# Kernel optimization log

Measured on AMD Instinct MI355X. Metric: run time of the kernel, lower is better.

## Reference

```python
import jax, jax.numpy as jnp
import numpy as np
from jax import lax

HIDDEN_DIM = 32
MLP_INNER = 8
VOCAB_SIZE = 64
INFERENCE_LR = 0.01
THRESHOLD = 4.0
B, L = 256, 4096
LN_EPS = 1e-5


def setup_inputs() -> dict:
    key = jax.random.key(0)
    ks = jax.random.split(key, 14)
    s = 0.1
    f32 = jnp.float32
    return {
        "seq": jax.random.randint(ks[0], (B, L), 0, VOCAB_SIZE),
        "embed": (jax.random.normal(ks[1], (VOCAB_SIZE, HIDDEN_DIM)) * s).astype(f32),
        "ff1_w": (jax.random.normal(ks[2], (2 * HIDDEN_DIM, HIDDEN_DIM)) * s).astype(f32),
        "ff1_b": jnp.zeros((2 * HIDDEN_DIM,), f32),
        "ff2_w": (jax.random.normal(ks[3], (HIDDEN_DIM, 2 * HIDDEN_DIM)) * s).astype(f32),
        "ff2_b": jnp.zeros((HIDDEN_DIM,), f32),
        "ln_g": jnp.ones((HIDDEN_DIM,), f32),
        "ln_b": jnp.zeros((HIDDEN_DIM,), f32),
        "fc1_w": (jax.random.normal(ks[4], (MLP_INNER, HIDDEN_DIM)) * s).astype(f32),
        "fc1_b": jnp.zeros((MLP_INNER,), f32),
        "fc2_w": (jax.random.normal(ks[5], (HIDDEN_DIM, MLP_INNER)) * s).astype(f32),
        "fc2_b": jnp.zeros((HIDDEN_DIM,), f32),
        "out_w": (jax.random.normal(ks[6], (VOCAB_SIZE, HIDDEN_DIM)) * s).astype(f32),
        "out_b": jnp.zeros((VOCAB_SIZE,), f32),
    }


def _encoder(seq, embed, ff1_w, ff1_b, ff2_w, ff2_b, ln_g, ln_b):
    h = embed[seq]  # [B, L, H]
    z = jax.nn.relu(jnp.einsum('blh,kh->blk', h, ff1_w) + ff1_b)
    f = jnp.einsum('blk,hk->blh', z, ff2_w) + ff2_b
    x = h + f
    mu = x.mean(-1, keepdims=True)
    var = ((x - mu) ** 2).mean(-1, keepdims=True)
    return ln_g * (x - mu) * lax.rsqrt(var + LN_EPS) + ln_b


def _fast_weight_scan(keys, vals, query, fc1_w, fc1_b, fc2_w, fc2_b):
    # keys, vals: [n_steps, H] for one sample; query: [H]
    H = keys.shape[-1]

    def step(carry, kv):
        W1, b1, W2, b2, ssum, cnt = carry
        k, v = kv
        mean_h = ssum / jnp.maximum(cnt, 1.0)
        dist = jnp.sqrt(jnp.sum((k - mean_h) ** 2))
        write = jnp.logical_or(cnt == 0.0, dist > THRESHOLD)
        # forward of tiny MLP on key
        z1 = W1 @ k + b1
        a = jax.nn.relu(z1)
        pred = W2 @ a + b2
        # MSE (mean over H) gradient, manual SGD step
        dpred = (2.0 / H) * (pred - v)
        dW2 = jnp.outer(dpred, a)
        db2 = dpred
        dz1 = (W2.T @ dpred) * (z1 > 0)
        dW1 = jnp.outer(dz1, k)
        db1 = dz1
        lr = INFERENCE_LR
        W1n = jnp.where(write, W1 - lr * dW1, W1)
        b1n = jnp.where(write, b1 - lr * db1, b1)
        W2n = jnp.where(write, W2 - lr * dW2, W2)
        b2n = jnp.where(write, b2 - lr * db2, b2)
        return (W1n, b1n, W2n, b2n, ssum + k, cnt + 1.0), write

    carry0 = (fc1_w, fc1_b, fc2_w, fc2_b, jnp.zeros_like(query), jnp.asarray(0.0, query.dtype))
    (W1, b1, W2, b2, _, _), writes = lax.scan(step, carry0, (keys, vals))
    context = W2 @ jax.nn.relu(W1 @ query + b1) + b2
    return context, writes.sum()


def reference(seq, embed, ff1_w, ff1_b, ff2_w, ff2_b, ln_g, ln_b,
              fc1_w, fc1_b, fc2_w, fc2_b, out_w, out_b):
    hidden = _encoder(seq, embed, ff1_w, ff1_b, ff2_w, ff2_b, ln_g, ln_b)
    hidden = lax.stop_gradient(hidden)  # inner loop uses detached hiddens
    Lseq = hidden.shape[1]
    n = (Lseq - 3 + 1) // 2  # len(range(0, L-3, 2))
    keys = hidden[:, 0:2 * n:2, :]   # [B, n, H]
    vals = hidden[:, 1:2 * n:2, :]   # [B, n, H]
    query = hidden[:, -1, :]          # [B, H]
    ctx, n_writes = jax.vmap(_fast_weight_scan, in_axes=(0, 0, 0, None, None, None, None))(
        keys, vals, query, fc1_w, fc1_b, fc2_w, fc2_b)
    ctx = lax.stop_gradient(ctx)  # torch computes context under no_grad
    logits = ctx @ out_w.T + out_b  # [B, VOCAB]
    write_rate = n_writes.sum().astype(jnp.float32) / (hidden.shape[0] * n)
    return logits, write_rate
```

## Files before the change

kernel.cpp:

```cpp
#include <hip/hip_runtime.h>

#define L_SEQ 4096
#define NSTEP 2047
#define ST_W  (-0.000625f)


__device__ __forceinline__ void redi4(float& a, float& b, float& c, float& d) {
    asm volatile(
        "s_nop 1\n\t"
        "v_add_f32_dpp %0, %0, %0 quad_perm:[1,0,3,2] row_mask:0xf bank_mask:0xf bound_ctrl:0\n\t"
        "v_add_f32_dpp %1, %1, %1 quad_perm:[1,0,3,2] row_mask:0xf bank_mask:0xf bound_ctrl:0\n\t"
        "v_add_f32_dpp %2, %2, %2 quad_perm:[1,0,3,2] row_mask:0xf bank_mask:0xf bound_ctrl:0\n\t"
        "v_add_f32_dpp %3, %3, %3 quad_perm:[1,0,3,2] row_mask:0xf bank_mask:0xf bound_ctrl:0\n\t"
        "v_add_f32_dpp %0, %0, %0 quad_perm:[2,3,0,1] row_mask:0xf bank_mask:0xf bound_ctrl:0\n\t"
        "v_add_f32_dpp %1, %1, %1 quad_perm:[2,3,0,1] row_mask:0xf bank_mask:0xf bound_ctrl:0\n\t"
        "v_add_f32_dpp %2, %2, %2 quad_perm:[2,3,0,1] row_mask:0xf bank_mask:0xf bound_ctrl:0\n\t"
        "v_add_f32_dpp %3, %3, %3 quad_perm:[2,3,0,1] row_mask:0xf bank_mask:0xf bound_ctrl:0\n\t"
        "v_add_f32_dpp %0, %0, %0 row_half_mirror row_mask:0xf bank_mask:0xf bound_ctrl:0\n\t"
        "v_add_f32_dpp %1, %1, %1 row_half_mirror row_mask:0xf bank_mask:0xf bound_ctrl:0\n\t"
        "v_add_f32_dpp %2, %2, %2 row_half_mirror row_mask:0xf bank_mask:0xf bound_ctrl:0\n\t"
        "v_add_f32_dpp %3, %3, %3 row_half_mirror row_mask:0xf bank_mask:0xf bound_ctrl:0"
        : "+v"(a), "+v"(b), "+v"(c), "+v"(d));
}

__device__ __forceinline__ float redg1(float x) {
    float t;
    asm volatile(
        "s_nop 1\n\t"
        "v_add_f32_dpp %0, %0, %0 row_ror:8 row_mask:0xf bank_mask:0xf bound_ctrl:0\n\t"
        "s_nop 1\n\t"
        "v_mov_b32 %1, %0\n\t"
        "s_nop 1\n\t"
        "v_permlane16_swap_b32 %1, %0\n\t"
        "s_nop 0\n\t"
        "v_add_f32 %0, %0, %1\n\t"
        "s_nop 1\n\t"
        "v_mov_b32 %1, %0\n\t"
        "s_nop 1\n\t"
        "v_permlane32_swap_b32 %1, %0\n\t"
        "s_nop 0\n\t"
        "v_add_f32 %0, %0, %1"
        : "+v"(x), "=&v"(t));
    return x;
}

__device__ __forceinline__ float sel8u(const float* Z, int r) {
    unsigned long long m0 = (r & 1) ? ~0ull : 0ull;
    unsigned long long m1 = (r & 2) ? ~0ull : 0ull;
    unsigned long long m2 = (r & 4) ? ~0ull : 0ull;
    float a0, a1, a2, a3, b0, b1v, res;
    asm("v_cndmask_b32 %0, %1, %2, %3" : "=v"(a0) : "v"(Z[0]), "v"(Z[1]), "s"(m0));
    asm("v_cndmask_b32 %0, %1, %2, %3" : "=v"(a1) : "v"(Z[2]), "v"(Z[3]), "s"(m0));
    asm("v_cndmask_b32 %0, %1, %2, %3" : "=v"(a2) : "v"(Z[4]), "v"(Z[5]), "s"(m0));
    asm("v_cndmask_b32 %0, %1, %2, %3" : "=v"(a3) : "v"(Z[6]), "v"(Z[7]), "s"(m0));
    asm("v_cndmask_b32 %0, %1, %2, %3" : "=v"(b0)  : "v"(a0), "v"(a1), "s"(m1));
    asm("v_cndmask_b32 %0, %1, %2, %3" : "=v"(b1v) : "v"(a2), "v"(a3), "s"(m1));
    asm("v_cndmask_b32 %0, %1, %2, %3" : "=v"(res) : "v"(b0), "v"(b1v), "s"(m2));
    return res;
}

__device__ __forceinline__ float bperm_row(int tok, int i4, float v) {
    int addr = ((tok & 56) << 2) | i4;
    return __int_as_float(__builtin_amdgcn_ds_bpermute(addr, __float_as_int(v)));
}

__device__ __forceinline__ int rli(int x, int l) {
    return __builtin_amdgcn_readlane(x, l);
}

__global__ __launch_bounds__(64) void build_kernel(
    const float* __restrict__ embed, const float* __restrict__ ff1_w,
    const float* __restrict__ ff1_b, const float* __restrict__ ff2_w,
    const float* __restrict__ ff2_b, const float* __restrict__ ln_g,
    const float* __restrict__ ln_b, const float* __restrict__ fc1_w,
    float* __restrict__ table, float* __restrict__ G, float* __restrict__ Z0)
{
    __shared__ float tl[64][32];
    const int v = threadIdx.x;
    float h[32], f[32];
#pragma unroll
    for (int j = 0; j < 32; ++j) { h[j] = embed[v * 32 + j]; f[j] = 0.f; }
    for (int k = 0; k < 64; ++k) {
        float z = ff1_b[k];
#pragma unroll
        for (int j = 0; j < 32; ++j) z += h[j] * ff1_w[k * 32 + j];
        z = fmaxf(z, 0.f);
#pragma unroll
        for (int j = 0; j < 32; ++j) f[j] += z * ff2_w[j * 64 + k];
    }
    float x[32], mu = 0.f;
#pragma unroll
    for (int j = 0; j < 32; ++j) { x[j] = h[j] + f[j] + ff2_b[j]; mu += x[j]; }
    mu *= (1.f / 32.f);
    float var = 0.f;
#pragma unroll
    for (int j = 0; j < 32; ++j) { float d = x[j] - mu; var += d * d; }
    var *= (1.f / 32.f);
    const float inv = rsqrtf(var + 1e-5f);
    float tv[32];
#pragma unroll
    for (int j = 0; j < 32; ++j) {
        tv[j] = ln_g[j] * (x[j] - mu) * inv + ln_b[j];
        tl[v][j] = tv[j];
        table[v * 32 + j] = tv[j];
    }
    __syncthreads();
    for (int u = 0; u < 64; ++u) {
        float acc = 0.f;
#pragma unroll
        for (int j = 0; j < 32; ++j) acc += tv[j] * tl[u][j];
        G[v * 64 + u] = acc;
    }
    for (int i = 0; i < 8; ++i) {
        float acc = 0.f;
#pragma unroll
        for (int j = 0; j < 32; ++j) acc += fc1_w[i * 32 + j] * tv[j];
        Z0[v * 8 + i] = acc;
    }
}

__global__ __launch_bounds__(256) void flags_kernel(
    const int* __restrict__ seq, const float* __restrict__ Gg,
    unsigned int* __restrict__ flags, float* __restrict__ wacc)
{
    __shared__ float Gs[4096];
    __shared__ float P[64][64];
    __shared__ int   kt[2048];
    __shared__ float Aa[2048];
    __shared__ float Ws[2048];
    __shared__ float red[256];
    const int tid = threadIdx.x, b = blockIdx.x;
    for (int idx = tid; idx < 4096; idx += 256) Gs[idx] = Gg[idx];
    const int2* sp2 = reinterpret_cast<const int2*>(seq + b * L_SEQ);
    for (int j = tid; j < 2048; j += 256) kt[j] = sp2[j].x;
    __syncthreads();

    for (int idx = tid; idx < 4096; idx += 256) {
        const int c = idx >> 6, u = idx & 63;
        const int base = c * 32;
        float s = 0.f;
#pragma unroll 4
        for (int j = 0; j < 32; ++j) s += Gs[kt[base + j] * 64 + u];
        P[c][u] = s;
    }
    __syncthreads();
    if (tid < 64) {
        float acc = 0.f;
        for (int c = 0; c < 64; ++c) { float p = P[c][tid]; P[c][tid] = acc; acc += p; }
    }
    __syncthreads();
    for (int t = tid; t < NSTEP; t += 256) {
        const int c = t >> 5, base = c << 5;
        const int ktt = kt[t];
        float a = P[c][ktt];
        for (int s = base; s < t; ++s) a += Gs[kt[s] * 64 + ktt];
        Aa[t] = a;
        Ws[t] = 2.f * a + Gs[ktt * 65];
    }
    __syncthreads();
    float loc[8], tot = 0.f;
    const int base8 = tid * 8;
#pragma unroll
    for (int j = 0; j < 8; ++j) {
        float v = (base8 + j < NSTEP) ? Ws[base8 + j] : 0.f;
        loc[j] = tot; tot += v;
    }
    red[tid] = tot;
    __syncthreads();
    float run = tot;
    for (int off = 1; off < 256; off <<= 1) {
        float add = (tid >= off) ? red[tid - off] : 0.f;
        __syncthreads();
        run += add; red[tid] = run;
        __syncthreads();
    }
    const float excl = run - tot;
    __syncthreads();
#pragma unroll
    for (int j = 0; j < 8; ++j) {
        const int t = base8 + j;
        if (t < NSTEP) {
            const float u_t = excl + loc[j];
            const float tf = (float)t;
            const int ktt = kt[t];
            const float r = fmaf(tf * tf, Gs[ktt * 65] - 16.f, u_t)
                            - 2.f * tf * Aa[t];
            Ws[t] = (t == 0 || r > 0.f) ? 1.f : 0.f;
        }
    }
    __syncthreads();
    int cnt = 0;
    if (tid < 64) {
        unsigned int w = 0;
        for (int j = 0; j < 32; ++j) {
            const int t = tid * 32 + j;
            if (t < NSTEP && Ws[t] != 0.f) w |= 1u << j;
        }
        flags[b * 64 + tid] = w;
        cnt = __popc(w);
    }
    red[tid] = (float)cnt;
    __syncthreads();
    if (tid == 0) {
        float s = 0.f;
        for (int j = 0; j < 64; ++j) s += red[j];
        atomicAdd(wacc, s);
    }
}

__global__ __launch_bounds__(64) void scan_kernel(
    const int* __restrict__ seq, const float* __restrict__ tableg,
    const float* __restrict__ Gg, const float* __restrict__ Z0g,
    const float* __restrict__ fc1_b, const float* __restrict__ fc2_w,
    const float* __restrict__ fc2_b, const float* __restrict__ out_w,
    const float* __restrict__ out_b, const unsigned int* __restrict__ flags,
    const float* __restrict__ wacc, float* __restrict__ out)
{
    __shared__ float Gs[4096];
    __shared__ float tabs[2048];
    __shared__ float ctx_s[32];
    const int b = blockIdx.x, tid = threadIdx.x;
    const int i = tid & 7, g = tid >> 3;
    const int l31 = tid & 31;
    const int i4 = i << 2;

    if (b == 0 && tid == 0) out[16384] = wacc[0] * (1.0f / 524032.0f);

    for (int idx = tid; idx < 4096; idx += 64) Gs[idx] = Gg[idx];
    for (int idx = tid; idx < 2048; idx += 64) tabs[idx] = tableg[idx];
    __syncthreads();
    const float4* tab4 = reinterpret_cast<const float4*>(tabs);

    float Zr[8];
#pragma unroll
    for (int r = 0; r < 8; ++r) Zr[r] = Z0g[(8 * g + r) * 8 + i];
    float b1 = fc1_b[i];
    float W2r0 = fc2_w[(4 * g + 0) * 8 + i];
    float W2r1 = fc2_w[(4 * g + 1) * 8 + i];
    float W2r2 = fc2_w[(4 * g + 2) * 8 + i];
    float W2r3 = fc2_w[(4 * g + 3) * 8 + i];
    float4 b2r = reinterpret_cast<const float4*>(fc2_b)[g];

    const int2* sp2 = reinterpret_cast<const int2*>(seq + b * L_SEQ);
    const unsigned int fwv = flags[b * 64 + tid];

    int2 cbA = sp2[l31];
    int2 cbB = sp2[32 + l31];
    int2 cbC = sp2[64 + l31];

    int k0t = rli(cbA.x, 0);
    int v0t = rli(cbA.y, 0);
    int kn1 = rli(cbA.x, 1);
    int vn1 = rli(cbA.y, 1);

    const float4* gp0 = reinterpret_cast<const float4*>(Gs + k0t * 64 + 8 * g);
    float4 GaC = gp0[0], GbC = gp0[1];
    float4 vc0 = tab4[v0t * 8 + g];
    float gbIn = Gs[k0t * 64 + kn1];
    float yb = bperm_row(k0t, i4, sel8u(Zr, k0t & 7)) + b1;
    float es0 = b2r.x - vc0.x, es1 = b2r.y - vc0.y;
    float es2 = b2r.z - vc0.z, es3 = b2r.w - vc0.w;
    float c_prev = 0.f, gB1c = 0.f;

    for (int c = 0; c < 64; ++c) {
        const unsigned int fw = (unsigned int)rli((int)fwv, c);
        {
            int c2 = c + 2; if (c2 > 63) c2 = 63;
            int2 t2 = sp2[c2 * 32 + l31];
            cbC = t2;
        }
#pragma unroll
        for (int j = 0; j < 32; ++j) {
            int kn2, vn2;
            if (j < 30) { kn2 = rli(cbA.x, j + 2); vn2 = rli(cbA.y, j + 2); }
            else        { kn2 = rli(cbB.x, j - 30); vn2 = rli(cbB.y, j - 30); }
            const float st = ((fw >> j) & 1u) ? ST_W : 0.f;

            float ynv = bperm_row(kn1, i4, sel8u(Zr, kn1 & 7));

            const float4* gpn =
                reinterpret_cast<const float4*>(Gs + kn1 * 64 + 8 * g);
            float4 GaN = gpn[0], GbN = gpn[1];
            float4 vcN = tab4[vn1 * 8 + g];
            float gbNew = Gs[kn1 * 64 + kn2];

            const float z1 = fmaf(c_prev, gB1c, yb);
            const float a  = fmaxf(z1, 0.f);
            float p0 = W2r0 * a, p1 = W2r1 * a, p2 = W2r2 * a, p3 = W2r3 * a;
            redi4(p0, p1, p2, p3);
            const float dp0 = p0 + es0, dp1 = p1 + es1;
            const float dp2 = p2 + es2, dp3 = p3 + es3;
            float q = redg1(fmaf(W2r0, dp0, W2r1 * dp1) +
                            fmaf(W2r2, dp2, W2r3 * dp3));
            const float cc = (z1 > 0.f) ? st * q : 0.f;

            const float u0 = st * dp0, u1 = st * dp1;
            const float u2 = st * dp2, u3 = st * dp3;
            W2r0 = fmaf(u0, a, W2r0); W2r1 = fmaf(u1, a, W2r1);
            W2r2 = fmaf(u2, a, W2r2); W2r3 = fmaf(u3, a, W2r3);
            b2r.x += u0; b2r.y += u1; b2r.z += u2; b2r.w += u3;
            Zr[0] = fmaf(cc, GaC.x, Zr[0]); Zr[1] = fmaf(cc, GaC.y, Zr[1]);
            Zr[2] = fmaf(cc, GaC.z, Zr[2]); Zr[3] = fmaf(cc, GaC.w, Zr[3]);
            Zr[4] = fmaf(cc, GbC.x, Zr[4]); Zr[5] = fmaf(cc, GbC.y, Zr[5]);
            Zr[6] = fmaf(cc, GbC.z, Zr[6]); Zr[7] = fmaf(cc, GbC.w, Zr[7]);
            const float ybN = ynv + b1;
            b1 += cc;
            es0 = b2r.x - vcN.x; es1 = b2r.y - vcN.y;
            es2 = b2r.z - vcN.z; es3 = b2r.w - vcN.w;

            yb = ybN; c_prev = cc; gB1c = gbIn + 1.f; gbIn = gbNew;
            GaC = GaN; GbC = GbN;
            kn1 = kn2; vn1 = vn2;
        }
        cbA = cbB; cbB = cbC;
    }

    const int tq = seq[b * L_SEQ + (L_SEQ - 1)];
    float yq = bperm_row(tq, i4, sel8u(Zr, tq & 7));
    const float zq = yq + b1;
    const float aq = fmaxf(zq, 0.f);
    float c0 = W2r0 * aq, c1 = W2r1 * aq, c2 = W2r2 * aq, c3 = W2r3 * aq;
    redi4(c0, c1, c2, c3);
    if (i == 0) {
        ctx_s[4 * g + 0] = c0 + b2r.x;
        ctx_s[4 * g + 1] = c1 + b2r.y;
        ctx_s[4 * g + 2] = c2 + b2r.z;
        ctx_s[4 * g + 3] = c3 + b2r.w;
    }
    __syncthreads();

    float acc = out_b[tid];
#pragma unroll
    for (int j = 0; j < 32; ++j) acc += ctx_s[j] * out_w[tid * 32 + j];
    out[b * 64 + tid] = acc;
}

extern "C" void kernel_launch(void* const* d_in, const int* in_sizes, int n_in,
                              void* d_out, int out_size, void* d_ws, size_t ws_size,
                              hipStream_t stream)
{
    const int*   seq   = (const int*)  d_in[0];
    const float* embed = (const float*)d_in[1];
    const float* ff1_w = (const float*)d_in[2];
    const float* ff1_b = (const float*)d_in[3];
    const float* ff2_w = (const float*)d_in[4];
    const float* ff2_b = (const float*)d_in[5];
    const float* ln_g  = (const float*)d_in[6];
    const float* ln_b  = (const float*)d_in[7];
    const float* fc1_w = (const float*)d_in[8];
    const float* fc1_b = (const float*)d_in[9];
    const float* fc2_w = (const float*)d_in[10];
    const float* fc2_b = (const float*)d_in[11];
    const float* out_w = (const float*)d_in[12];
    const float* out_b = (const float*)d_in[13];

    float* out = (float*)d_out;
    char* ws = (char*)d_ws;
    float*        table = (float*)(ws + 0);
    float*        G     = (float*)(ws + 8192);
    float*        Z0    = (float*)(ws + 24576);
    float*        wacc  = (float*)(ws + 26624);
    unsigned int* flags = (unsigned int*)(ws + 28672);

    hipMemsetAsync(wacc, 0, sizeof(float), stream);
    hipLaunchKernelGGL(build_kernel, dim3(1), dim3(64), 0, stream,
                       embed, ff1_w, ff1_b, ff2_w, ff2_b, ln_g, ln_b, fc1_w,
                       table, G, Z0);
    hipLaunchKernelGGL(flags_kernel, dim3(256), dim3(256), 0, stream,
                       seq, G, flags, wacc);
    hipLaunchKernelGGL(scan_kernel, dim3(256), dim3(64), 0, stream,
                       seq, table, G, Z0, fc1_b, fc2_w, fc2_b,
                       out_w, out_b, flags, wacc, out);
}
```

Before: 472.3 us.

## Fuse table/Gram build into flags kernel and shorten scan prefetch distance

Removes the single-block build kernel and has every flags_kernel block recompute the 64-entry LayerNorm table and the Gram matrix in shared memory, with block 0 writing table, G and Z0 to global memory for the scan kernel. This drops one serial launch that ran on a single wave and the global reload of G. The scan loop's lookahead on next token ids is cut from two steps to one, which removes a carried register pair but exposes the LDS loads for the next step with less lead time. Each flags block now repeats the small encoder MLP work, adding redundant compute per block.

```diff
diff --git a/kernel.cpp b/kernel.cpp
--- a/kernel.cpp
+++ b/kernel.cpp
@@ -68,71 +68,74 @@
     return __builtin_amdgcn_readlane(x, l);
 }
 
-__global__ __launch_bounds__(64) void build_kernel(
-    const float* __restrict__ embed, const float* __restrict__ ff1_w,
-    const float* __restrict__ ff1_b, const float* __restrict__ ff2_w,
-    const float* __restrict__ ff2_b, const float* __restrict__ ln_g,
-    const float* __restrict__ ln_b, const float* __restrict__ fc1_w,
-    float* __restrict__ table, float* __restrict__ G, float* __restrict__ Z0)
-{
-    __shared__ float tl[64][32];
-    const int v = threadIdx.x;
-    float h[32], f[32];
-#pragma unroll
-    for (int j = 0; j < 32; ++j) { h[j] = embed[v * 32 + j]; f[j] = 0.f; }
-    for (int k = 0; k < 64; ++k) {
-        float z = ff1_b[k];
-#pragma unroll
-        for (int j = 0; j < 32; ++j) z += h[j] * ff1_w[k * 32 + j];
-        z = fmaxf(z, 0.f);
-#pragma unroll
-        for (int j = 0; j < 32; ++j) f[j] += z * ff2_w[j * 64 + k];
-    }
-    float x[32], mu = 0.f;
-#pragma unroll
-    for (int j = 0; j < 32; ++j) { x[j] = h[j] + f[j] + ff2_b[j]; mu += x[j]; }
-    mu *= (1.f / 32.f);
-    float var = 0.f;
-#pragma unroll
-    for (int j = 0; j < 32; ++j) { float d = x[j] - mu; var += d * d; }
-    var *= (1.f / 32.f);
-    const float inv = rsqrtf(var + 1e-5f);
-    float tv[32];
-#pragma unroll
-    for (int j = 0; j < 32; ++j) {
-        tv[j] = ln_g[j] * (x[j] - mu) * inv + ln_b[j];
-        tl[v][j] = tv[j];
-        table[v * 32 + j] = tv[j];
-    }
-    __syncthreads();
-    for (int u = 0; u < 64; ++u) {
-        float acc = 0.f;
-#pragma unroll
-        for (int j = 0; j < 32; ++j) acc += tv[j] * tl[u][j];
-        G[v * 64 + u] = acc;
-    }
-    for (int i = 0; i < 8; ++i) {
-        float acc = 0.f;
-#pragma unroll
-        for (int j = 0; j < 32; ++j) acc += fc1_w[i * 32 + j] * tv[j];
-        Z0[v * 8 + i] = acc;
-    }
-}
-
 __global__ __launch_bounds__(256) void flags_kernel(
-    const int* __restrict__ seq, const float* __restrict__ Gg,
+    const int* __restrict__ seq, const float* __restrict__ embed,
+    const float* __restrict__ ff1_w, const float* __restrict__ ff1_b,
+    const float* __restrict__ ff2_w, const float* __restrict__ ff2_b,
+    const float* __restrict__ ln_g, const float* __restrict__ ln_b,
+    const float* __restrict__ fc1_w,
+    float* __restrict__ table, float* __restrict__ G, float* __restrict__ Z0,
     unsigned int* __restrict__ flags, float* __restrict__ wacc)
 {
     __shared__ float Gs[4096];
+    __shared__ float tl[64][32];
     __shared__ float P[64][64];
     __shared__ int   kt[2048];
     __shared__ float Aa[2048];
     __shared__ float Ws[2048];
     __shared__ float red[256];
     const int tid = threadIdx.x, b = blockIdx.x;
-    for (int idx = tid; idx < 4096; idx += 256) Gs[idx] = Gg[idx];
     const int2* sp2 = reinterpret_cast<const int2*>(seq + b * L_SEQ);
     for (int j = tid; j < 2048; j += 256) kt[j] = sp2[j].x;
+
+    if (tid < 64) {
+        const int v = tid;
+        float h[32], f[32];
+#pragma unroll
+        for (int j = 0; j < 32; ++j) { h[j] = embed[v * 32 + j]; f[j] = 0.f; }
+        for (int k = 0; k < 64; ++k) {
+            float z = ff1_b[k];
+#pragma unroll
+            for (int j = 0; j < 32; ++j) z += h[j] * ff1_w[k * 32 + j];
+            z = fmaxf(z, 0.f);
+#pragma unroll
+            for (int j = 0; j < 32; ++j) f[j] += z * ff2_w[j * 64 + k];
+        }
+        float x[32], mu = 0.f;
+#pragma unroll
+        for (int j = 0; j < 32; ++j) { x[j] = h[j] + f[j] + ff2_b[j]; mu += x[j]; }
+        mu *= (1.f / 32.f);
+        float var = 0.f;
+#pragma unroll
+        for (int j = 0; j < 32; ++j) { float d = x[j] - mu; var += d * d; }
+        var *= (1.f / 32.f);
+        const float inv = rsqrtf(var + 1e-5f);
+#pragma unroll
+        for (int j = 0; j < 32; ++j) {
+            float tv = ln_g[j] * (x[j] - mu) * inv + ln_b[j];
+            tl[v][j] = tv;
+            if (b == 0) table[v * 32 + j] = tv;
+        }
+    }
+    __syncthreads();
+
+    for (int idx = tid; idx < 4096; idx += 256) {
+        const int v = idx >> 6, u = idx & 63;
+        float acc = 0.f;
+#pragma unroll
+        for (int j = 0; j < 32; ++j) acc += tl[v][j] * tl[u][j];
+        Gs[idx] = acc;
+        if (b == 0) G[idx] = acc;
+    }
+    if (b == 0) {
+        for (int idx = tid; idx < 512; idx += 256) {
+            const int v = idx >> 3, i = idx & 7;
+            float acc = 0.f;
+#pragma unroll
+            for (int j = 0; j < 32; ++j) acc += fc1_w[i * 32 + j] * tl[v][j];
+            Z0[idx] = acc;
+        }
+    }
     __syncthreads();
 
     for (int idx = tid; idx < 4096; idx += 256) {
@@ -246,18 +249,14 @@
 
     int2 cbA = sp2[l31];
     int2 cbB = sp2[32 + l31];
-    int2 cbC = sp2[64 + l31];
-
-    int k0t = rli(cbA.x, 0);
-    int v0t = rli(cbA.y, 0);
-    int kn1 = rli(cbA.x, 1);
-    int vn1 = rli(cbA.y, 1);
-
-    const float4* gp0 = reinterpret_cast<const float4*>(Gs + k0t * 64 + 8 * g);
+    int2 cbC;
+
+    int kS = rli(cbA.x, 0);
+    int vS = rli(cbA.y, 0);
+    const float4* gp0 = reinterpret_cast<const float4*>(Gs + kS * 64 + 8 * g);
     float4 GaC = gp0[0], GbC = gp0[1];
-    float4 vc0 = tab4[v0t * 8 + g];
-    float gbIn = Gs[k0t * 64 + kn1];
-    float yb = bperm_row(k0t, i4, sel8u(Zr, k0t & 7)) + b1;
+    float4 vc0 = tab4[vS * 8 + g];
+    float yb = bperm_row(kS, i4, sel8u(Zr, kS & 7)) + b1;
     float es0 = b2r.x - vc0.x, es1 = b2r.y - vc0.y;
     float es2 = b2r.z - vc0.z, es3 = b2r.w - vc0.w;
     float c_prev = 0.f, gB1c = 0.f;
@@ -266,23 +265,21 @@
         const unsigned int fw = (unsigned int)rli((int)fwv, c);
         {
             int c2 = c + 2; if (c2 > 63) c2 = 63;
-            int2 t2 = sp2[c2 * 32 + l31];
-            cbC = t2;
+            cbC = sp2[c2 * 32 + l31];
         }
 #pragma unroll
         for (int j = 0; j < 32; ++j) {
-            int kn2, vn2;
-            if (j < 30) { kn2 = rli(cbA.x, j + 2); vn2 = rli(cbA.y, j + 2); }
-            else        { kn2 = rli(cbB.x, j - 30); vn2 = rli(cbB.y, j - 30); }
+            int kN, vN;
+            if (j < 31) { kN = rli(cbA.x, j + 1); vN = rli(cbA.y, j + 1); }
+            else        { kN = rli(cbB.x, 0);     vN = rli(cbB.y, 0); }
             const float st = ((fw >> j) & 1u) ? ST_W : 0.f;
 
-            float ynv = bperm_row(kn1, i4, sel8u(Zr, kn1 & 7));
-
+            float ynv = bperm_row(kN, i4, sel8u(Zr, kN & 7));
             const float4* gpn =
-                reinterpret_cast<const float4*>(Gs + kn1 * 64 + 8 * g);
+                reinterpret_cast<const float4*>(Gs + kN * 64 + 8 * g);
             float4 GaN = gpn[0], GbN = gpn[1];
-            float4 vcN = tab4[vn1 * 8 + g];
-            float gbNew = Gs[kn1 * 64 + kn2];
+            float4 vcN = tab4[vN * 8 + g];
+            float gbN = Gs[kS * 64 + kN];
 
             const float z1 = fmaf(c_prev, gB1c, yb);
             const float a  = fmaxf(z1, 0.f);
@@ -308,9 +305,8 @@
             es0 = b2r.x - vcN.x; es1 = b2r.y - vcN.y;
             es2 = b2r.z - vcN.z; es3 = b2r.w - vcN.w;
 
-            yb = ybN; c_prev = cc; gB1c = gbIn + 1.f; gbIn = gbNew;
-            GaC = GaN; GbC = GbN;
-            kn1 = kn2; vn1 = vn2;
+            yb = ybN; c_prev = cc; gB1c = gbN + 1.f;
+            GaC = GaN; GbC = GbN; kS = kN;
         }
         cbA = cbB; cbB = cbC;
     }
@@ -363,11 +359,9 @@
     unsigned int* flags = (unsigned int*)(ws + 28672);
 
     hipMemsetAsync(wacc, 0, sizeof(float), stream);
-    hipLaunchKernelGGL(build_kernel, dim3(1), dim3(64), 0, stream,
-                       embed, ff1_w, ff1_b, ff2_w, ff2_b, ln_g, ln_b, fc1_w,
-                       table, G, Z0);
     hipLaunchKernelGGL(flags_kernel, dim3(256), dim3(256), 0, stream,
-                       seq, G, flags, wacc);
+                       seq, embed, ff1_w, ff1_b, ff2_w, ff2_b, ln_g, ln_b,
+                       fc1_w, table, G, Z0, flags, wacc);
     hipLaunchKernelGGL(scan_kernel, dim3(256), dim3(64), 0, stream,
                        seq, table, G, Z0, fc1_b, fc2_w, fc2_b,
                        out_w, out_b, flags, wacc, out);
```

Measured after the change: 465.5 us. About the same (-1.4%).
